# Optimization experiments

Measured on AMD Instinct MI355X. Metric: run time of the kernel, lower is better.

## Reference

```python
import jax, jax.numpy as jnp
import numpy as np

N_NODES = 100000
N_EDGES = 1600000
IN_CH = 128
OUT_CH = 32
HID = 2 * OUT_CH


def setup_inputs() -> dict:
    key = jax.random.key(0)
    k1, k2, k3, k4 = jax.random.split(key, 4)
    x = jax.random.normal(k1, (N_NODES, IN_CH), dtype=jnp.float32)
    edge_index = jax.random.randint(k2, (2, N_EDGES), 0, N_NODES, dtype=jnp.int64)
    W1 = jax.random.normal(k3, (IN_CH, HID), dtype=jnp.float32) / np.sqrt(IN_CH)
    b1 = jnp.zeros((HID,), dtype=jnp.float32)
    W2 = jax.random.normal(k4, (HID, OUT_CH), dtype=jnp.float32) / np.sqrt(HID)
    b2 = jnp.zeros((OUT_CH,), dtype=jnp.float32)
    return {"x": x, "edge_index": edge_index, "W1": W1, "b1": b1, "W2": W2, "b2": b2}


def _gcn_norm(edge_index, n_nodes):
    # GCNConv default: add self-loops, symmetric deg^{-1/2} normalization.
    loop = jnp.arange(n_nodes, dtype=edge_index.dtype)
    src = jnp.concatenate([edge_index[0], loop])
    dst = jnp.concatenate([edge_index[1], loop])
    deg = jax.ops.segment_sum(jnp.ones_like(dst, dtype=jnp.float32), dst, num_segments=n_nodes)
    dinv = jnp.where(deg > 0, jax.lax.rsqrt(deg), 0.0)
    norm = dinv[src] * dinv[dst]  # [E + N]
    return src, dst, norm


def _gcn_conv(h, W, b, src, dst, norm, n_nodes):
    m = h @ W                      # transform first (small GEMM)
    msg = m[src] * norm[:, None]   # gather + scale per edge
    agg = jax.ops.segment_sum(msg, dst, num_segments=n_nodes)  # scatter-add
    return agg + b


def reference(x, edge_index, W1, b1, W2, b2):
    n = x.shape[0]
    src, dst, norm = _gcn_norm(edge_index, n)
    h = jax.nn.relu(_gcn_conv(x, W1, b1, src, dst, norm, n))
    return _gcn_conv(h, W2, b2, src, dst, norm, n)
```

## Files before the change

kernel.cpp:

```cpp
#include <hip/hip_runtime.h>

#define IN_CH 128
#define HID 64
#define OUT_CH 32
#define BUCKET_CAP 6144
#define NB_MAX 512

typedef _Float16 f16x8 __attribute__((ext_vector_type(8)));
typedef float f32x4 __attribute__((ext_vector_type(4)));

__device__ __forceinline__ unsigned short f32_to_bf16(float f) {
    union { float f; unsigned int u; } v; v.f = f;
    unsigned int u = v.u;
    u += 0x7FFFu + ((u >> 16) & 1u);
    return (unsigned short)(u >> 16);
}
__device__ __forceinline__ float bf16_to_f32(unsigned short h) {
    union { unsigned int u; float f; } v; v.u = ((unsigned int)h) << 16;
    return v.f;
}
__device__ __forceinline__ float bf16_lo(unsigned int u) {
    union { unsigned int u; float f; } v; v.u = u << 16; return v.f;
}
__device__ __forceinline__ float bf16_hi(unsigned int u) {
    union { unsigned int u; float f; } v; v.u = u & 0xFFFF0000u; return v.f;
}

__device__ __forceinline__ int load_idx(const void* e, long long i, int is64) {
    if (is64) return ((const int*)e)[2 * i];
    return ((const int*)e)[i];
}

__global__ __launch_bounds__(256) void binA_kernel(
    const void* __restrict__ edges, long long E,
    int* __restrict__ bucket_cur, unsigned int* __restrict__ entries, int nb) {
    __shared__ int hist[NB_MAX];
    __shared__ int cbase[NB_MAX];
    __shared__ int s_is64;
    const int tid = threadIdx.x;

    if (tid < 64) {
        int v = ((const int*)edges)[2 * tid + 1];
        unsigned long long nz = __ballot(v != 0);
        if (tid == 0) s_is64 = (nz == 0ull) ? 1 : 0;
    }
    for (int i = tid; i < nb; i += 256) hist[i] = 0;
    __syncthreads();
    const int is64 = s_is64;

    const long long per = (E + gridDim.x - 1) / gridDim.x;
    const long long lo = blockIdx.x * per;
    const long long hi = (lo + per < E) ? lo + per : E;

    for (long long i = lo + tid; i < hi; i += 256) {
        int dst = load_idx(edges, E + i, is64);
        atomicAdd(&hist[dst >> 8], 1);
    }
    __syncthreads();
    for (int i = tid; i < nb; i += 256) {
        int c = hist[i];
        int base = (c > 0) ? atomicAdd(&bucket_cur[i], c) : 0;
        cbase[i] = base;
        hist[i] = 0;
    }
    __syncthreads();
    for (long long i = lo + tid; i < hi; i += 256) {
        int src = load_idx(edges, i, is64);
        int dst = load_idx(edges, E + i, is64);
        int b = dst >> 8;
        int rel = cbase[b] + atomicAdd(&hist[b], 1);
        if (rel < BUCKET_CAP)
            entries[(long long)b * BUCKET_CAP + rel] = ((unsigned)src << 8) | (unsigned)(dst & 255);
    }
}

__global__ __launch_bounds__(256) void binB1_kernel(
    const unsigned int* __restrict__ entries, const int* __restrict__ bucket_cur,
    int* __restrict__ counts, int* __restrict__ row_off, float* __restrict__ dinv,
    int n) {
    __shared__ int hist[256];
    __shared__ int scan[256];
    const int b   = blockIdx.x;
    const int tid = threadIdx.x;
    const long long seg = (long long)b * BUCKET_CAP;
    int cnt = bucket_cur[b];
    if (cnt > BUCKET_CAP) cnt = BUCKET_CAP;

    hist[tid] = 0;
    __syncthreads();
    for (int i = tid; i < cnt; i += 256)
        atomicAdd(&hist[entries[seg + i] & 255], 1);
    __syncthreads();

    int v = hist[tid];
    scan[tid] = v;
    __syncthreads();
    for (int off = 1; off < 256; off <<= 1) {
        int t = (tid >= off) ? scan[tid - off] : 0;
        __syncthreads();
        scan[tid] += t;
        __syncthreads();
    }
    int ex = scan[tid] - v;
    int node = (b << 8) + tid;
    if (node < n) {
        counts[node]  = v;
        row_off[node] = (int)seg + ex;
        dinv[node]    = rsqrtf((float)v + 1.0f);
    }
}

__global__ __launch_bounds__(256) void binB2_kernel(
    const unsigned int* __restrict__ entries, const int* __restrict__ bucket_cur,
    const int* __restrict__ row_off, const float* __restrict__ dinv,
    int2* __restrict__ ew, int n) {
    __shared__ int cur[256];
    __shared__ float ldi[256];
    const int b   = blockIdx.x;
    const int tid = threadIdx.x;
    const long long seg = (long long)b * BUCKET_CAP;
    int cnt = bucket_cur[b];
    if (cnt > BUCKET_CAP) cnt = BUCKET_CAP;

    int node = (b << 8) + tid;
    cur[tid] = (node < n) ? row_off[node] - (int)seg : 0;
    ldi[tid] = (node < n) ? dinv[node] : 0.f;
    __syncthreads();

    for (int i = tid; i < cnt; i += 256) {
        unsigned e = entries[seg + i];
        int d = (int)(e & 255u);
        int s = (int)(e >> 8);
        int r = atomicAdd(&cur[d], 1);
        float w = dinv[s] * ldi[d];
        int2 o; o.x = s; o.y = __float_as_int(w);
        ew[seg + r] = o;
    }
}

__global__ __launch_bounds__(256) void gemm1_kernel(
    const float* __restrict__ x, const float* __restrict__ W1,
    unsigned short* __restrict__ m1bf, int n) {
    const int lane = threadIdx.x & 63;
    const int wid  = threadIdx.x >> 6;
    const int m    = lane & 15;
    const int g    = lane >> 4;
    const int Rw   = blockIdx.x * 64 + wid * 16;

    f16x8 wf[4][4];
#pragma unroll
    for (int t = 0; t < 4; ++t) {
        const float* wp = W1 + (t * 32 + g * 8) * HID + m;
#pragma unroll
        for (int c = 0; c < 4; ++c) {
#pragma unroll
            for (int j = 0; j < 8; ++j)
                wf[c][t][j] = (_Float16)wp[j * HID + c * 16];
        }
    }

    int rl = Rw + m;
    if (rl >= n) rl = n - 1;
    const float* xr = x + (long long)rl * IN_CH;

    f32x4 acc[4] = {};

#pragma unroll
    for (int t = 0; t < 4; ++t) {
        float4 xa = *(const float4*)(xr + t * 32 + g * 8);
        float4 xb = *(const float4*)(xr + t * 32 + g * 8 + 4);
        f16x8 af;
        af[0] = (_Float16)xa.x; af[1] = (_Float16)xa.y;
        af[2] = (_Float16)xa.z; af[3] = (_Float16)xa.w;
        af[4] = (_Float16)xb.x; af[5] = (_Float16)xb.y;
        af[6] = (_Float16)xb.z; af[7] = (_Float16)xb.w;
#pragma unroll
        for (int c = 0; c < 4; ++c)
            acc[c] = __builtin_amdgcn_mfma_f32_16x16x32_f16(af, wf[c][t], acc[c], 0, 0, 0);
    }

#pragma unroll
    for (int c = 0; c < 4; ++c) {
#pragma unroll
        for (int r = 0; r < 4; ++r) {
            int row = Rw + g * 4 + r;
            if (row < n)
                m1bf[(long long)row * HID + c * 16 + m] = f32_to_bf16(acc[c][r]);
        }
    }
}

#define PADH 132
__global__ __launch_bounds__(256) void gemm2_kernel(
    const unsigned short* __restrict__ hbf, const float* __restrict__ W2,
    unsigned short* __restrict__ m2bf, int n) {
    __shared__ __align__(16) float sW[HID * OUT_CH];
    __shared__ __align__(16) float sH[HID * PADH];
    const int tid = threadIdx.x;

    {
        const float4* Wv = (const float4*)W2;
        float4* sWv = (float4*)sW;
        for (int i = tid; i < HID * OUT_CH / 4; i += 256) sWv[i] = Wv[i];
    }

    const int R0 = blockIdx.x * 128;
    for (int i = tid; i < 128 * 8; i += 256) {
        int r = i >> 3;
        int q = i & 7;
        int row = R0 + r;
        uint4 v = make_uint4(0u, 0u, 0u, 0u);
        if (row < n)
            v = ((const uint4*)(hbf + (long long)row * HID))[q];
        int k0 = q * 8;
        sH[(k0 + 0) * PADH + r] = bf16_lo(v.x);
        sH[(k0 + 1) * PADH + r] = bf16_hi(v.x);
        sH[(k0 + 2) * PADH + r] = bf16_lo(v.y);
        sH[(k0 + 3) * PADH + r] = bf16_hi(v.y);
        sH[(k0 + 4) * PADH + r] = bf16_lo(v.z);
        sH[(k0 + 5) * PADH + r] = bf16_hi(v.z);
        sH[(k0 + 6) * PADH + r] = bf16_lo(v.w);
        sH[(k0 + 7) * PADH + r] = bf16_hi(v.w);
    }
    __syncthreads();

    const int tx = tid & 7;
    const int ty = tid >> 3;
    float acc[4][4] = {};
    const float* pH = sH + ty * 4;
    const float* pW = sW + tx * 4;
#pragma unroll 8
    for (int k = 0; k < HID; ++k) {
        float4 hv = *(const float4*)(pH + k * PADH);
        float4 wv = *(const float4*)(pW + k * OUT_CH);
        acc[0][0] += hv.x * wv.x; acc[0][1] += hv.x * wv.y;
        acc[0][2] += hv.x * wv.z; acc[0][3] += hv.x * wv.w;
        acc[1][0] += hv.y * wv.x; acc[1][1] += hv.y * wv.y;
        acc[1][2] += hv.y * wv.z; acc[1][3] += hv.y * wv.w;
        acc[2][0] += hv.z * wv.x; acc[2][1] += hv.z * wv.y;
        acc[2][2] += hv.z * wv.z; acc[2][3] += hv.z * wv.w;
        acc[3][0] += hv.w * wv.x; acc[3][1] += hv.w * wv.y;
        acc[3][2] += hv.w * wv.z; acc[3][3] += hv.w * wv.w;
    }

#pragma unroll
    for (int i = 0; i < 4; ++i) {
        int row = R0 + ty * 4 + i;
        if (row < n) {
            ushort4 o;
            o.x = f32_to_bf16(acc[i][0]);
            o.y = f32_to_bf16(acc[i][1]);
            o.z = f32_to_bf16(acc[i][2]);
            o.w = f32_to_bf16(acc[i][3]);
            *(ushort4*)(m2bf + (long long)row * OUT_CH + tx * 4) = o;
        }
    }
}

__global__ __launch_bounds__(256) void gather64_kernel(
    const int* __restrict__ row_off, const int* __restrict__ counts,
    const int2* __restrict__ ew, const float* __restrict__ dinv,
    const unsigned short* __restrict__ m1bf, const float* __restrict__ b1,
    unsigned short* __restrict__ hbf, int n) {
    int node = blockIdx.x * 4 + (threadIdx.x >> 6);
    int lane = threadIdx.x & 63;
    if (node >= n) return;
    int start = __builtin_amdgcn_readfirstlane(row_off[node]);
    int cnt   = __builtin_amdgcn_readfirstlane(counts[node]);
    const int eg = lane >> 4;
    const int q  = lane & 15;

    float a0 = 0.f, a1 = 0.f, a2 = 0.f, a3 = 0.f;
    int j = 0;
    for (; j + 7 < cnt; j += 8) {
        int2 ea = ew[start + j + eg];
        int2 eb = ew[start + j + 4 + eg];
        uint2 va = *(const uint2*)(m1bf + (unsigned)(ea.x * HID) + q * 4);
        uint2 vb = *(const uint2*)(m1bf + (unsigned)(eb.x * HID) + q * 4);
        float wa = __int_as_float(ea.y);
        float wb = __int_as_float(eb.y);
        a0 += bf16_lo(va.x) * wa; a1 += bf16_hi(va.x) * wa;
        a2 += bf16_lo(va.y) * wa; a3 += bf16_hi(va.y) * wa;
        a0 += bf16_lo(vb.x) * wb; a1 += bf16_hi(vb.x) * wb;
        a2 += bf16_lo(vb.y) * wb; a3 += bf16_hi(vb.y) * wb;
    }
    for (; j < cnt; j += 4) {
        int idx  = j + eg;
        int cidx = (idx < cnt) ? idx : cnt - 1;
        int2 e = ew[start + cidx];
        float w = (idx < cnt) ? __int_as_float(e.y) : 0.f;
        uint2 v = *(const uint2*)(m1bf + (unsigned)(e.x * HID) + q * 4);
        a0 += bf16_lo(v.x) * w; a1 += bf16_hi(v.x) * w;
        a2 += bf16_lo(v.y) * w; a3 += bf16_hi(v.y) * w;
    }

    a0 += __shfl_xor(a0, 16, 64); a1 += __shfl_xor(a1, 16, 64);
    a2 += __shfl_xor(a2, 16, 64); a3 += __shfl_xor(a3, 16, 64);
    a0 += __shfl_xor(a0, 32, 64); a1 += __shfl_xor(a1, 32, 64);
    a2 += __shfl_xor(a2, 32, 64); a3 += __shfl_xor(a3, 32, 64);

    if (lane < 16) {
        float dd = dinv[node];
        float ss = dd * dd;
        uint2 sv = *(const uint2*)(m1bf + (unsigned)(node * HID) + lane * 4);
        float4 bv = *(const float4*)(b1 + lane * 4);
        ushort4 o;
        o.x = f32_to_bf16(fmaxf(a0 + bf16_lo(sv.x) * ss + bv.x, 0.f));
        o.y = f32_to_bf16(fmaxf(a1 + bf16_hi(sv.x) * ss + bv.y, 0.f));
        o.z = f32_to_bf16(fmaxf(a2 + bf16_lo(sv.y) * ss + bv.z, 0.f));
        o.w = f32_to_bf16(fmaxf(a3 + bf16_hi(sv.y) * ss + bv.w, 0.f));
        *(ushort4*)(hbf + (unsigned)(node * HID) + lane * 4) = o;
    }
}

__global__ __launch_bounds__(256) void gather32_kernel(
    const int* __restrict__ row_off, const int* __restrict__ counts,
    const int2* __restrict__ ew, const float* __restrict__ dinv,
    const unsigned short* __restrict__ m2bf, const float* __restrict__ b2,
    float* __restrict__ out, int n) {
    int node = blockIdx.x * 4 + (threadIdx.x >> 6);
    int lane = threadIdx.x & 63;
    if (node >= n) return;
    int start = __builtin_amdgcn_readfirstlane(row_off[node]);
    int cnt   = __builtin_amdgcn_readfirstlane(counts[node]);
    const int eg = lane >> 3;
    const int q  = lane & 7;

    float a0 = 0.f, a1 = 0.f, a2 = 0.f, a3 = 0.f;
    int j = 0;
    for (; j + 15 < cnt; j += 16) {
        int2 ea = ew[start + j + eg];
        int2 eb = ew[start + j + 8 + eg];
        uint2 va = *(const uint2*)(m2bf + (unsigned)(ea.x * OUT_CH) + q * 4);
        uint2 vb = *(const uint2*)(m2bf + (unsigned)(eb.x * OUT_CH) + q * 4);
        float wa = __int_as_float(ea.y);
        float wb = __int_as_float(eb.y);
        a0 += bf16_lo(va.x) * wa; a1 += bf16_hi(va.x) * wa;
        a2 += bf16_lo(va.y) * wa; a3 += bf16_hi(va.y) * wa;
        a0 += bf16_lo(vb.x) * wb; a1 += bf16_hi(vb.x) * wb;
        a2 += bf16_lo(vb.y) * wb; a3 += bf16_hi(vb.y) * wb;
    }
    for (; j < cnt; j += 8) {
        int idx  = j + eg;
        int cidx = (idx < cnt) ? idx : cnt - 1;
        int2 e = ew[start + cidx];
        float w = (idx < cnt) ? __int_as_float(e.y) : 0.f;
        uint2 v = *(const uint2*)(m2bf + (unsigned)(e.x * OUT_CH) + q * 4);
        a0 += bf16_lo(v.x) * w; a1 += bf16_hi(v.x) * w;
        a2 += bf16_lo(v.y) * w; a3 += bf16_hi(v.y) * w;
    }

    a0 += __shfl_xor(a0,  8, 64); a1 += __shfl_xor(a1,  8, 64);
    a2 += __shfl_xor(a2,  8, 64); a3 += __shfl_xor(a3,  8, 64);
    a0 += __shfl_xor(a0, 16, 64); a1 += __shfl_xor(a1, 16, 64);
    a2 += __shfl_xor(a2, 16, 64); a3 += __shfl_xor(a3, 16, 64);
    a0 += __shfl_xor(a0, 32, 64); a1 += __shfl_xor(a1, 32, 64);
    a2 += __shfl_xor(a2, 32, 64); a3 += __shfl_xor(a3, 32, 64);

    if (lane < 8) {
        float dd = dinv[node];
        float ss = dd * dd;
        uint2 sv = *(const uint2*)(m2bf + (unsigned)(node * OUT_CH) + lane * 4);
        float4 bv = *(const float4*)(b2 + lane * 4);
        float4 o;
        o.x = a0 + bf16_lo(sv.x) * ss + bv.x;
        o.y = a1 + bf16_hi(sv.x) * ss + bv.y;
        o.z = a2 + bf16_lo(sv.y) * ss + bv.z;
        o.w = a3 + bf16_hi(sv.y) * ss + bv.w;
        *(float4*)(out + (unsigned)(node * OUT_CH) + lane * 4) = o;
    }
}

extern "C" void kernel_launch(void* const* d_in, const int* in_sizes, int n_in,
                              void* d_out, int out_size, void* d_ws, size_t ws_size,
                              hipStream_t stream) {
    const float* x     = (const float*)d_in[0];
    const void*  edges = d_in[1];
    const float* W1    = (const float*)d_in[2];
    const float* b1    = (const float*)d_in[3];
    const float* W2    = (const float*)d_in[4];
    const float* b2    = (const float*)d_in[5];
    float* out = (float*)d_out;

    const int n = in_sizes[0] / IN_CH;
    const long long E = (long long)in_sizes[1] / 2;
    const int nb = (n + 255) / 256;

    float* ws         = (float*)d_ws;
    float* dinv       = ws;
    unsigned short* m1bf = (unsigned short*)(ws + n);
    unsigned short* m2bf = m1bf;
    float* agg        = ws + n + (long long)n * HID / 2;
    unsigned int* entries = (unsigned int*)agg;
    unsigned short* hbf   = (unsigned short*)agg;
    int*   counts     = (int*)(agg + (long long)n * HID);
    int*   row_off    = counts + n;
    int*   bucket_cur = row_off + n;
    int2*  ew         = (int2*)(bucket_cur + NB_MAX);

    hipMemsetAsync(bucket_cur, 0, NB_MAX * sizeof(int), stream);

    binA_kernel<<<256, 256, 0, stream>>>(edges, E, bucket_cur, entries, nb);
    binB1_kernel<<<nb, 256, 0, stream>>>(entries, bucket_cur, counts, row_off, dinv, n);
    binB2_kernel<<<nb, 256, 0, stream>>>(entries, bucket_cur, row_off, dinv, ew, n);

    gemm1_kernel<<<(n + 63) / 64, 256, 0, stream>>>(x, W1, m1bf, n);
    gather64_kernel<<<(n + 3) / 4, 256, 0, stream>>>(
        row_off, counts, ew, dinv, m1bf, b1, hbf, n);

    gemm2_kernel<<<(n + 127) / 128, 256, 0, stream>>>(hbf, W2, m2bf, n);
    gather32_kernel<<<(n + 3) / 4, 256, 0, stream>>>(
        row_off, counts, ew, dinv, m2bf, b2, out, n);
}
```

Baseline: 266.5 us.

## Co-schedule edge binning with first GEMM in one launch; unroll gather by 16

Merges the edge-binning kernel and the first feature-transform GEMM into a single launch, where the first 256 blocks bin edges and the remaining blocks run the MFMA GEMM. The two pieces of work are independent, so they can overlap and one launch is saved. The 64-wide gather loop is also unrolled from 8 to 16 edges per iteration to keep more loads in flight. In exchange, shared memory for the binning path is reserved by every block, which may lower GEMM occupancy, and the larger unroll uses more registers.

```diff
diff --git a/kernel.cpp b/kernel.cpp
--- a/kernel.cpp
+++ b/kernel.cpp
@@ -5,6 +5,7 @@
 #define OUT_CH 32
 #define BUCKET_CAP 6144
 #define NB_MAX 512
+#define NBA 256
 
 typedef _Float16 f16x8 __attribute__((ext_vector_type(8)));
 typedef float f32x4 __attribute__((ext_vector_type(4)));
@@ -31,46 +32,101 @@
     return ((const int*)e)[i];
 }
 
-__global__ __launch_bounds__(256) void binA_kernel(
+__global__ __launch_bounds__(256) void fusedA_kernel(
     const void* __restrict__ edges, long long E,
-    int* __restrict__ bucket_cur, unsigned int* __restrict__ entries, int nb) {
-    __shared__ int hist[NB_MAX];
-    __shared__ int cbase[NB_MAX];
-    __shared__ int s_is64;
+    int* __restrict__ bucket_cur, unsigned int* __restrict__ entries, int nb,
+    const float* __restrict__ x, const float* __restrict__ W1,
+    unsigned short* __restrict__ m1bf, int n) {
     const int tid = threadIdx.x;
 
-    if (tid < 64) {
-        int v = ((const int*)edges)[2 * tid + 1];
-        unsigned long long nz = __ballot(v != 0);
-        if (tid == 0) s_is64 = (nz == 0ull) ? 1 : 0;
-    }
-    for (int i = tid; i < nb; i += 256) hist[i] = 0;
-    __syncthreads();
-    const int is64 = s_is64;
-
-    const long long per = (E + gridDim.x - 1) / gridDim.x;
-    const long long lo = blockIdx.x * per;
-    const long long hi = (lo + per < E) ? lo + per : E;
-
-    for (long long i = lo + tid; i < hi; i += 256) {
-        int dst = load_idx(edges, E + i, is64);
-        atomicAdd(&hist[dst >> 8], 1);
-    }
-    __syncthreads();
-    for (int i = tid; i < nb; i += 256) {
-        int c = hist[i];
-        int base = (c > 0) ? atomicAdd(&bucket_cur[i], c) : 0;
-        cbase[i] = base;
-        hist[i] = 0;
-    }
-    __syncthreads();
-    for (long long i = lo + tid; i < hi; i += 256) {
-        int src = load_idx(edges, i, is64);
-        int dst = load_idx(edges, E + i, is64);
-        int b = dst >> 8;
-        int rel = cbase[b] + atomicAdd(&hist[b], 1);
-        if (rel < BUCKET_CAP)
-            entries[(long long)b * BUCKET_CAP + rel] = ((unsigned)src << 8) | (unsigned)(dst & 255);
+    if (blockIdx.x < NBA) {
+        __shared__ int hist[NB_MAX];
+        __shared__ int cbase[NB_MAX];
+        __shared__ int s_is64;
+
+        if (tid < 64) {
+            int v = ((const int*)edges)[2 * tid + 1];
+            unsigned long long nz = __ballot(v != 0);
+            if (tid == 0) s_is64 = (nz == 0ull) ? 1 : 0;
+        }
+        for (int i = tid; i < nb; i += 256) hist[i] = 0;
+        __syncthreads();
+        const int is64 = s_is64;
+
+        const long long per = (E + NBA - 1) / NBA;
+        const long long lo = blockIdx.x * per;
+        const long long hi = (lo + per < E) ? lo + per : E;
+
+        for (long long i = lo + tid; i < hi; i += 256) {
+            int dst = load_idx(edges, E + i, is64);
+            atomicAdd(&hist[dst >> 8], 1);
+        }
+        __syncthreads();
+        for (int i = tid; i < nb; i += 256) {
+            int c = hist[i];
+            int base = (c > 0) ? atomicAdd(&bucket_cur[i], c) : 0;
+            cbase[i] = base;
+            hist[i] = 0;
+        }
+        __syncthreads();
+        for (long long i = lo + tid; i < hi; i += 256) {
+            int src = load_idx(edges, i, is64);
+            int dst = load_idx(edges, E + i, is64);
+            int b = dst >> 8;
+            int rel = cbase[b] + atomicAdd(&hist[b], 1);
+            if (rel < BUCKET_CAP)
+                entries[(long long)b * BUCKET_CAP + rel] =
+                    ((unsigned)src << 8) | (unsigned)(dst & 255);
+        }
+    } else {
+        const int bix  = blockIdx.x - NBA;
+        const int lane = tid & 63;
+        const int wid  = tid >> 6;
+        const int m    = lane & 15;
+        const int g    = lane >> 4;
+        const int Rw   = bix * 64 + wid * 16;
+
+        f16x8 wf[4][4];
+#pragma unroll
+        for (int t = 0; t < 4; ++t) {
+            const float* wp = W1 + (t * 32 + g * 8) * HID + m;
+#pragma unroll
+            for (int c = 0; c < 4; ++c) {
+#pragma unroll
+                for (int j = 0; j < 8; ++j)
+                    wf[c][t][j] = (_Float16)wp[j * HID + c * 16];
+            }
+        }
+
+        int rl = Rw + m;
+        if (rl >= n) rl = n - 1;
+        const float* xr = x + (long long)rl * IN_CH;
+
+        f32x4 acc[4] = {};
+
+#pragma unroll
+        for (int t = 0; t < 4; ++t) {
+            float4 xa = *(const float4*)(xr + t * 32 + g * 8);
+            float4 xb = *(const float4*)(xr + t * 32 + g * 8 + 4);
+            f16x8 af;
+            af[0] = (_Float16)xa.x; af[1] = (_Float16)xa.y;
+            af[2] = (_Float16)xa.z; af[3] = (_Float16)xa.w;
+            af[4] = (_Float16)xb.x; af[5] = (_Float16)xb.y;
+            af[6] = (_Float16)xb.z; af[7] = (_Float16)xb.w;
+#pragma unroll
+            for (int c = 0; c < 4; ++c)
+                acc[c] = __builtin_amdgcn_mfma_f32_16x16x32_f16(af, wf[c][t], acc[c], 0, 0, 0);
+        }
+
+#pragma unroll
+        for (int c = 0; c < 4; ++c) {
+#pragma unroll
+            for (int r = 0; r < 4; ++r) {
+                int row = Rw + g * 4 + r;
+                if (row < n)
+                    m1bf[(long long)row * HID + c * 16 + m] = f32_to_bf16(acc[c][r]);
+            }
+        }
     }
 }
 
@@ -135,58 +191,6 @@
         float w = dinv[s] * ldi[d];
         int2 o; o.x = s; o.y = __float_as_int(w);
         ew[seg + r] = o;
-    }
-}
-
-__global__ __launch_bounds__(256) void gemm1_kernel(
-    const float* __restrict__ x, const float* __restrict__ W1,
-    unsigned short* __restrict__ m1bf, int n) {
-    const int lane = threadIdx.x & 63;
-    const int wid  = threadIdx.x >> 6;
-    const int m    = lane & 15;
-    const int g    = lane >> 4;
-    const int Rw   = blockIdx.x * 64 + wid * 16;
-
-    f16x8 wf[4][4];
-#pragma unroll
-    for (int t = 0; t < 4; ++t) {
-        const float* wp = W1 + (t * 32 + g * 8) * HID + m;
-#pragma unroll
-        for (int c = 0; c < 4; ++c) {
-#pragma unroll
-            for (int j = 0; j < 8; ++j)
-                wf[c][t][j] = (_Float16)wp[j * HID + c * 16];
-        }
-    }
-
-    int rl = Rw + m;
-    if (rl >= n) rl = n - 1;
-    const float* xr = x + (long long)rl * IN_CH;
-
-    f32x4 acc[4] = {};
-
-#pragma unroll
-    for (int t = 0; t < 4; ++t) {
-        float4 xa = *(const float4*)(xr + t * 32 + g * 8);
-        float4 xb = *(const float4*)(xr + t * 32 + g * 8 + 4);
-        f16x8 af;
-        af[0] = (_Float16)xa.x; af[1] = (_Float16)xa.y;
-        af[2] = (_Float16)xa.z; af[3] = (_Float16)xa.w;
-        af[4] = (_Float16)xb.x; af[5] = (_Float16)xb.y;
-        af[6] = (_Float16)xb.z; af[7] = (_Float16)xb.w;
-#pragma unroll
-        for (int c = 0; c < 4; ++c)
-            acc[c] = __builtin_amdgcn_mfma_f32_16x16x32_f16(af, wf[c][t], acc[c], 0, 0, 0);
-    }
-
-#pragma unroll
-    for (int c = 0; c < 4; ++c) {
-#pragma unroll
-        for (int r = 0; r < 4; ++r) {
-            int row = Rw + g * 4 + r;
-            if (row < n)
-                m1bf[(long long)row * HID + c * 16 + m] = f32_to_bf16(acc[c][r]);
-        }
     }
 }
 
@@ -272,17 +276,27 @@
 
     float a0 = 0.f, a1 = 0.f, a2 = 0.f, a3 = 0.f;
     int j = 0;
-    for (; j + 7 < cnt; j += 8) {
-        int2 ea = ew[start + j + eg];
-        int2 eb = ew[start + j + 4 + eg];
-        uint2 va = *(const uint2*)(m1bf + (unsigned)(ea.x * HID) + q * 4);
-        uint2 vb = *(const uint2*)(m1bf + (unsigned)(eb.x * HID) + q * 4);
-        float wa = __int_as_float(ea.y);
-        float wb = __int_as_float(eb.y);
-        a0 += bf16_lo(va.x) * wa; a1 += bf16_hi(va.x) * wa;
-        a2 += bf16_lo(va.y) * wa; a3 += bf16_hi(va.y) * wa;
-        a0 += bf16_lo(vb.x) * wb; a1 += bf16_hi(vb.x) * wb;
-        a2 += bf16_lo(vb.y) * wb; a3 += bf16_hi(vb.y) * wb;
+    for (; j + 15 < cnt; j += 16) {
+        int2 e0 = ew[start + j      + eg];
+        int2 e1 = ew[start + j + 4  + eg];
+        int2 e2 = ew[start + j + 8  + eg];
+        int2 e3 = ew[start + j + 12 + eg];
+        uint2 v0 = *(const uint2*)(m1bf + (unsigned)(e0.x * HID) + q * 4);
+        uint2 v1 = *(const uint2*)(m1bf + (unsigned)(e1.x * HID) + q * 4);
+        uint2 v2 = *(const uint2*)(m1bf + (unsigned)(e2.x * HID) + q * 4);
+        uint2 v3 = *(const uint2*)(m1bf + (unsigned)(e3.x * HID) + q * 4);
+        float w0 = __int_as_float(e0.y);
+        float w1 = __int_as_float(e1.y);
+        float w2 = __int_as_float(e2.y);
+        float w3 = __int_as_float(e3.y);
+        a0 += bf16_lo(v0.x) * w0; a1 += bf16_hi(v0.x) * w0;
+        a2 += bf16_lo(v0.y) * w0; a3 += bf16_hi(v0.y) * w0;
+        a0 += bf16_lo(v1.x) * w1; a1 += bf16_hi(v1.x) * w1;
+        a2 += bf16_lo(v1.y) * w1; a3 += bf16_hi(v1.y) * w1;
+        a0 += bf16_lo(v2.x) * w2; a1 += bf16_hi(v2.x) * w2;
+        a2 += bf16_lo(v2.y) * w2; a3 += bf16_hi(v2.y) * w2;
+        a0 += bf16_lo(v3.x) * w3; a1 += bf16_hi(v3.x) * w3;
+        a2 += bf16_lo(v3.y) * w3; a3 += bf16_hi(v3.y) * w3;
     }
     for (; j < cnt; j += 4) {
         int idx  = j + eg;
@@ -400,11 +414,13 @@
 
     hipMemsetAsync(bucket_cur, 0, NB_MAX * sizeof(int), stream);
 
-    binA_kernel<<<256, 256, 0, stream>>>(edges, E, bucket_cur, entries, nb);
+    const int gemm1_blocks = (n + 63) / 64;
+    fusedA_kernel<<<NBA + gemm1_blocks, 256, 0, stream>>>(
+        edges, E, bucket_cur, entries, nb, x, W1, m1bf, n);
+
     binB1_kernel<<<nb, 256, 0, stream>>>(entries, bucket_cur, counts, row_off, dinv, n);
     binB2_kernel<<<nb, 256, 0, stream>>>(entries, bucket_cur, row_off, dinv, ew, n);
 
-    gemm1_kernel<<<(n + 63) / 64, 256, 0, stream>>>(x, W1, m1bf, n);
     gather64_kernel<<<(n + 3) / 4, 256, 0, stream>>>(
         row_off, counts, ew, dinv, m1bf, b1, hbf, n);
 
```

Result: no change. 263.0 us (-1.3%).
